# Kernel optimization log

Measured on AMD Instinct MI355X. Metric: run time of the kernel, lower is better.

Reference implementation:

```python
import jax, jax.numpy as jnp
import numpy as np
import math

S, B, D, H = 2048, 2, 1024, 16
DK = D // H

def setup_inputs() -> dict:
    key = jax.random.key(0)
    ks = jax.random.split(key, 32)
    f = lambda k, shape, s=1.0: jax.random.normal(k, shape, dtype=jnp.float32) * s
    inp = {
        'qx': f(ks[0], (S, B, D)),
        'kx': f(ks[1], (S, B, D)),
        'vx': f(ks[2], (S, B, D)),
        'qc': f(ks[3], (S, B, D)),
        'kc': f(ks[4], (S, B, D)),
    }
    w = 1.0 / math.sqrt(D)
    names = ['qx_lin', 'kx_lin', 'vx_lin', 'qc_lin', 'kc_lin', 'out_lin']
    for i, n in enumerate(names):
        inp['W_' + n] = f(ks[5 + 2 * i], (D, D), w)
        inp['b_' + n] = f(ks[6 + 2 * i], (D,), w)
    vnames = ['Vqx', 'Vqc', 'Vkx', 'Vkc']
    for i, n in enumerate(vnames):
        inp['W_' + n] = f(ks[17 + 2 * i], (D, 1), w)
        inp['b_' + n] = f(ks[18 + 2 * i], (1,), w)
    return inp

def _forward(qx, kx, vx, qc, kc,
             W_qx_lin, b_qx_lin, W_kx_lin, b_kx_lin, W_vx_lin, b_vx_lin,
             W_qc_lin, b_qc_lin, W_kc_lin, b_kc_lin, W_out_lin, b_out_lin,
             W_Vqx, b_Vqx, W_Vqc, b_Vqc, W_Vkx, b_Vkx, W_Vkc, b_Vkc):
    # [S,B,D] -> [B,S,D]
    qx = jnp.swapaxes(qx, 0, 1)
    kx = jnp.swapaxes(kx, 0, 1)
    vx = jnp.swapaxes(vx, 0, 1)
    qc = jnp.swapaxes(qc, 0, 1)
    kc = jnp.swapaxes(kc, 0, 1)
    bs = qx.shape[0]

    qx = qx @ W_qx_lin + b_qx_lin
    kx = kx @ W_kx_lin + b_kx_lin
    v = vx @ W_vx_lin + b_vx_lin
    qc = qc @ W_qc_lin + b_qc_lin
    kc = kc @ W_kc_lin + b_kc_lin

    lam_q = jax.nn.sigmoid((qx @ W_Vqx + b_Vqx) + (qc @ W_Vqc + b_Vqc))  # [B,S,1]
    lam_k = jax.nn.sigmoid((kx @ W_Vkx + b_Vkx) + (kc @ W_Vkc + b_Vkc))
    q = (1.0 - lam_q) * qx + lam_q * qc
    k = (1.0 - lam_k) * kx + lam_k * kc

    # [B,S,D] -> [B,H,S,dk]
    q = q.reshape(bs, -1, H, DK).transpose(0, 2, 1, 3)
    k = k.reshape(bs, -1, H, DK).transpose(0, 2, 1, 3)
    v = v.reshape(bs, -1, H, DK).transpose(0, 2, 1, 3)

    scores = jnp.einsum('bhqd,bhkd->bhqk', q, k) / math.sqrt(DK)
    attn = jax.nn.softmax(scores, axis=-1)  # dropout is identity in eval
    ctx = jnp.einsum('bhqk,bhkd->bhqd', attn, v)

    concat = ctx.transpose(0, 2, 1, 3).reshape(bs, -1, D)
    out = concat @ W_out_lin + b_out_lin
    return jnp.swapaxes(out, 0, 1)  # back to [S,B,D]

def reference(qx, kx, vx, qc, kc,
              W_qx_lin, b_qx_lin, W_kx_lin, b_kx_lin, W_vx_lin, b_vx_lin,
              W_qc_lin, b_qc_lin, W_kc_lin, b_kc_lin, W_out_lin, b_out_lin,
              W_Vqx, b_Vqx, W_Vqc, b_Vqc, W_Vkx, b_Vkx, W_Vkc, b_Vkc):
    return _forward(qx, kx, vx, qc, kc,
                    W_qx_lin, b_qx_lin, W_kx_lin, b_kx_lin, W_vx_lin, b_vx_lin,
                    W_qc_lin, b_qc_lin, W_kc_lin, b_kc_lin, W_out_lin, b_out_lin,
                    W_Vqx, b_Vqx, W_Vqc, b_Vqc, W_Vkx, b_Vkx, W_Vkc, b_Vkc)
```

## Files before the change

### kernel.cpp

```cpp
#include <hip/hip_runtime.h>
#include <math.h>

typedef unsigned short u16;
typedef __attribute__((ext_vector_type(8))) short short8;
typedef __attribute__((ext_vector_type(4))) float floatx4;
typedef __attribute__((ext_vector_type(4))) unsigned short ushort4v;
typedef __attribute__((ext_vector_type(2))) unsigned int uint2v;

__device__ __forceinline__ float bf2f(u16 x) {
    union { unsigned int u; float f; } v; v.u = ((unsigned int)x) << 16; return v.f;
}
__device__ __forceinline__ u16 f2bf(float f) {
    union { float f; unsigned int u; } v; v.f = f;
    unsigned int r = v.u + 0x7fffu + ((v.u >> 16) & 1u);
    return (u16)(r >> 16);
}
__device__ __forceinline__ unsigned int pk2bf(float a, float b) {
#if __has_builtin(__builtin_amdgcn_cvt_pk_bf16_f32)
    auto r = __builtin_amdgcn_cvt_pk_bf16_f32(a, b);
    union { decltype(r) v; unsigned int u; } cv; cv.v = r; return cv.u;
#else
    return (unsigned int)f2bf(a) | ((unsigned int)f2bf(b) << 16);
#endif
}

__device__ __forceinline__ void gl_lds16(const void* g, void* l) {
    __builtin_amdgcn_global_load_lds(
        (const __attribute__((address_space(1))) unsigned int*)g,
        (__attribute__((address_space(3))) unsigned int*)l,
        16, 0, 0);
}

struct WFuseJobs { const float* W[4]; const float* wv[4]; float* out[4]; };

__global__ __launch_bounds__(256) void wfuse(WFuseJobs wf) {
    const int z = blockIdx.y;
    const float* W = wf.W[z];
    const float* wv = wf.wv[z];
    float* out = wf.out[z];
    const int lane = threadIdx.x & 63, w = threadIdx.x >> 6;
#pragma unroll
    for (int i = 0; i < 4; i++) {
        const int row = blockIdx.x * 16 + w * 4 + i;
        const float* Wr = W + (size_t)row * 1024 + lane * 16;
        const float* vr = wv + lane * 16;
        float p = 0.f;
#pragma unroll
        for (int c = 0; c < 4; c++) {
            const floatx4 a = *(const floatx4*)(Wr + c * 4);
            const floatx4 b = *(const floatx4*)(vr + c * 4);
            p += a[0] * b[0] + a[1] * b[1] + a[2] * b[2] + a[3] * b[3];
        }
#pragma unroll
        for (int m = 1; m <= 32; m <<= 1) p += __shfl_xor(p, m);
        if (lane == 0) out[row] = p;
    }
}

struct CastJobs { const float* src[5]; u16* dst[5]; const float* w[5]; float* dot[5]; };

__global__ __launch_bounds__(256) void castbf(CastJobs cj) {
    const int z = blockIdx.y;
    const int row = blockIdx.x;
    const int t = threadIdx.x;
    const size_t i = (size_t)row * 256 + t;
    const floatx4 v = *(const floatx4*)(cj.src[z] + i * 4);
    ushort4v o;
#pragma unroll
    for (int j = 0; j < 4; j++) o[j] = f2bf(v[j]);
    *(ushort4v*)(cj.dst[z] + i * 4) = o;

    if (cj.w[z]) {
        const floatx4 wv = *(const floatx4*)(cj.w[z] + t * 4);
        float p = v[0] * wv[0] + v[1] * wv[1] + v[2] * wv[2] + v[3] * wv[3];
#pragma unroll
        for (int m = 1; m <= 32; m <<= 1) p += __shfl_xor(p, m);
        __shared__ float red[4];
        if ((t & 63) == 0) red[t >> 6] = p;
        __syncthreads();
        if (t == 0) cj.dot[z][row] = red[0] + red[1] + red[2] + red[3];
    }
}

struct LamJobs {
    const float* dA[2]; const float* dB[2];
    const float* b1[2]; const float* b2[2];
    const float* wv1[2]; const float* wv2[2];
    const float* s1[2]; const float* s2[2];
    float* lam[2];
};

__global__ __launch_bounds__(256) void lamk(LamJobs lj) {
    const int z = blockIdx.y;
    const int t = threadIdx.x;
    float p = 0.f;
    {
        const floatx4 a1 = *(const floatx4*)(lj.b1[z] + t * 4);
        const floatx4 w1 = *(const floatx4*)(lj.wv1[z] + t * 4);
        const floatx4 a2 = *(const floatx4*)(lj.b2[z] + t * 4);
        const floatx4 w2 = *(const floatx4*)(lj.wv2[z] + t * 4);
#pragma unroll
        for (int j = 0; j < 4; j++) p += a1[j] * w1[j] + a2[j] * w2[j];
    }
#pragma unroll
    for (int m = 1; m <= 32; m <<= 1) p += __shfl_xor(p, m);
    __shared__ float red[4];
    if ((t & 63) == 0) red[t >> 6] = p;
    __syncthreads();
    const float c = red[0] + red[1] + red[2] + red[3] + lj.s1[z][0] + lj.s2[z][0];
    const int row = blockIdx.x * 256 + t;
    const float x = lj.dA[z][row] + lj.dB[z][row] + c;
    lj.lam[z][row] = 1.f / (1.f + exp2f(-x * 1.44269504f));
}

struct WTJobs { const float* src[6]; u16* dst[6]; };

__global__ __launch_bounds__(256) void wtrans(WTJobs wj) {
    __shared__ float tile[32][33];
    const int z = blockIdx.z;
    const float* W = wj.src[z];
    u16* Wt = wj.dst[z];
    const int n0 = blockIdx.x * 32, k0 = blockIdx.y * 32;
    const int tx = threadIdx.x & 31, ty = threadIdx.x >> 5;
#pragma unroll
    for (int i = 0; i < 4; i++)
        tile[ty + i * 8][tx] = W[(size_t)(k0 + ty + i * 8) * 1024 + n0 + tx];
    __syncthreads();
#pragma unroll
    for (int i = 0; i < 4; i++)
        Wt[(size_t)(n0 + ty + i * 8) * 1024 + k0 + tx] = f2bf(tile[tx][ty + i * 8]);
}

__global__ __launch_bounds__(256) void vtrans(const u16* __restrict__ V,
                                              u16* __restrict__ Vtg) {
    __shared__ u16 tile[32][34];
    const int bh = blockIdx.z, b = bh >> 4, h = bh & 15;
    const int base = b * 1024 + h * 64;
    const int s0 = blockIdx.x * 32, d0 = blockIdx.y * 32;
    const int tx = threadIdx.x & 31, ty = threadIdx.x >> 5;
#pragma unroll
    for (int i = 0; i < 4; i++)
        tile[ty + i * 8][tx] = V[(size_t)(s0 + ty + i * 8) * 2048 + base + d0 + tx];
    __syncthreads();
#pragma unroll
    for (int i = 0; i < 4; i++)
        Vtg[((size_t)bh * 64 + d0 + ty + i * 8) * 2048 + s0 + tx] = tile[tx][ty + i * 8];
}

struct GemmJob { const u16* A; const u16* Bt; const float* bias; u16* Cb; float* Cf; };
struct GemmJobs { GemmJob j[1]; };

__global__ __launch_bounds__(256, 2) void gemm_bt(GemmJobs jobs, int K, int N, int f32out) {
    __shared__ u16 As[128 * 32];
    __shared__ u16 Bs[128 * 32];
    const GemmJob jb = jobs.j[blockIdx.z];
    const int m0 = blockIdx.y * 128;
    const int n0 = blockIdx.x * 128;
    const int t = threadIdx.x;
    const int lane = t & 63;
    const int wid = t >> 6;
    const int wm = wid >> 1, wn = wid & 1;
    const int qd = lane >> 4, lm = lane & 15;

    const floatx4 zero4 = {0.f, 0.f, 0.f, 0.f};
    floatx4 acc[4][4];
#pragma unroll
    for (int i = 0; i < 4; i++)
#pragma unroll
        for (int j2 = 0; j2 < 4; j2++) acc[i][j2] = zero4;

    const u16* Ab = jb.A + (size_t)m0 * K;
    const u16* Bb = jb.Bt + (size_t)n0 * K;
    const int e0 = t * 8;
    const int r0 = e0 >> 5, c0 = e0 & 31;
    const int e1 = (256 + t) * 8;
    const int r1 = e1 >> 5, c1 = e1 & 31;

    for (int k0 = 0; k0 < K; k0 += 32) {
        __syncthreads();
        gl_lds16(Ab + (size_t)r0 * K + k0 + c0, &As[e0]);
        gl_lds16(Ab + (size_t)r1 * K + k0 + c1, &As[e1]);
        gl_lds16(Bb + (size_t)r0 * K + k0 + c0, &Bs[e0]);
        gl_lds16(Bb + (size_t)r1 * K + k0 + c1, &Bs[e1]);
        __syncthreads();

        short8 af[4], bfg[4];
#pragma unroll
        for (int i = 0; i < 4; i++) {
            af[i]  = *(const short8*)&As[(wm * 64 + i * 16 + lm) * 32 + qd * 8];
            bfg[i] = *(const short8*)&Bs[(wn * 64 + i * 16 + lm) * 32 + qd * 8];
        }
#pragma unroll
        for (int i = 0; i < 4; i++)
#pragma unroll
            for (int j2 = 0; j2 < 4; j2++)
                acc[i][j2] = __builtin_amdgcn_mfma_f32_16x16x32_bf16(af[i], bfg[j2], acc[i][j2], 0, 0, 0);
    }

#pragma unroll
    for (int i = 0; i < 4; i++) {
        const int mb = m0 + wm * 64 + i * 16 + qd * 4;
#pragma unroll
        for (int j2 = 0; j2 < 4; j2++) {
            const int col = n0 + wn * 64 + j2 * 16 + lm;
            const float bv = jb.bias[col];
            const floatx4 c = acc[i][j2];
            if (f32out) {
#pragma unroll
                for (int r = 0; r < 4; r++)
                    jb.Cf[(size_t)(mb + r) * N + col] = c[r] + bv;
            } else {
#pragma unroll
                for (int r = 0; r < 4; r++)
                    jb.Cb[(size_t)(mb + r) * N + col] = f2bf(c[r] + bv);
            }
        }
    }
}

struct FuseJob {
    const u16* Aa; const u16* Ac; const u16* Ba; const u16* Bc;
    const float* biasA; const float* biasC; const float* lam; u16* out;
};
struct FuseJobs { FuseJob j[2]; };

__global__ __launch_bounds__(256, 2) void fusedproj(FuseJobs jobs) {
    __shared__ u16 Asa[128 * 32];
    __shared__ u16 Asc[128 * 32];
    __shared__ u16 Bsa[128 * 32];
    __shared__ u16 Bsc[128 * 32];
    const FuseJob jb = jobs.j[blockIdx.z];
    const int K = 1024;
    const int m0 = blockIdx.y * 128;
    const int n0 = blockIdx.x * 128;
    const int t = threadIdx.x;
    const int lane = t & 63;
    const int wid = t >> 6;
    const int wm = wid >> 1, wn = wid & 1;
    const int qd = lane >> 4, lm = lane & 15;

    const floatx4 zero4 = {0.f, 0.f, 0.f, 0.f};
    floatx4 accA[4][4], accC[4][4];
#pragma unroll
    for (int i = 0; i < 4; i++)
#pragma unroll
        for (int j2 = 0; j2 < 4; j2++) { accA[i][j2] = zero4; accC[i][j2] = zero4; }

    const u16* Aab = jb.Aa + (size_t)m0 * K;
    const u16* Acb = jb.Ac + (size_t)m0 * K;
    const u16* Bab = jb.Ba + (size_t)n0 * K;
    const u16* Bcb = jb.Bc + (size_t)n0 * K;
    const int e0 = t * 8;
    const int r0 = e0 >> 5, c0 = e0 & 31;
    const int e1 = (256 + t) * 8;
    const int r1 = e1 >> 5, c1 = e1 & 31;

    for (int k0 = 0; k0 < K; k0 += 32) {
        __syncthreads();
        gl_lds16(Aab + (size_t)r0 * K + k0 + c0, &Asa[e0]);
        gl_lds16(Aab + (size_t)r1 * K + k0 + c1, &Asa[e1]);
        gl_lds16(Acb + (size_t)r0 * K + k0 + c0, &Asc[e0]);
        gl_lds16(Acb + (size_t)r1 * K + k0 + c1, &Asc[e1]);
        gl_lds16(Bab + (size_t)r0 * K + k0 + c0, &Bsa[e0]);
        gl_lds16(Bab + (size_t)r1 * K + k0 + c1, &Bsa[e1]);
        gl_lds16(Bcb + (size_t)r0 * K + k0 + c0, &Bsc[e0]);
        gl_lds16(Bcb + (size_t)r1 * K + k0 + c1, &Bsc[e1]);
        __syncthreads();

        short8 aa[4], ac[4], ba[4], bc[4];
#pragma unroll
        for (int i = 0; i < 4; i++) {
            aa[i] = *(const short8*)&Asa[(wm * 64 + i * 16 + lm) * 32 + qd * 8];
            ac[i] = *(const short8*)&Asc[(wm * 64 + i * 16 + lm) * 32 + qd * 8];
            ba[i] = *(const short8*)&Bsa[(wn * 64 + i * 16 + lm) * 32 + qd * 8];
            bc[i] = *(const short8*)&Bsc[(wn * 64 + i * 16 + lm) * 32 + qd * 8];
        }
#pragma unroll
        for (int i = 0; i < 4; i++)
#pragma unroll
            for (int j2 = 0; j2 < 4; j2++) {
                accA[i][j2] = __builtin_amdgcn_mfma_f32_16x16x32_bf16(aa[i], ba[j2], accA[i][j2], 0, 0, 0);
                accC[i][j2] = __builtin_amdgcn_mfma_f32_16x16x32_bf16(ac[i], bc[j2], accC[i][j2], 0, 0, 0);
            }
    }

#pragma unroll
    for (int i = 0; i < 4; i++) {
        const int mb = m0 + wm * 64 + i * 16 + qd * 4;
        float lamv[4];
#pragma unroll
        for (int r = 0; r < 4; r++) lamv[r] = jb.lam[mb + r];
#pragma unroll
        for (int j2 = 0; j2 < 4; j2++) {
            const int col = n0 + wn * 64 + j2 * 16 + lm;
            const float bA = jb.biasA[col];
            const float bC = jb.biasC[col];
#pragma unroll
            for (int r = 0; r < 4; r++) {
                const float va = accA[i][j2][r] + bA;
                const float vc = accC[i][j2][r] + bC;
                jb.out[(size_t)(mb + r) * 1024 + col] = f2bf(va + lamv[r] * (vc - va));
            }
        }
    }
}

__global__ __launch_bounds__(256, 2) void attn3(
    const u16* __restrict__ Q, const u16* __restrict__ Kk,
    const u16* __restrict__ Vtg, float* __restrict__ ctxp,
    float* __restrict__ lp) {
    __shared__ u16 Ks[64 * 72];
    __shared__ u16 Vs[64 * 72];
    __shared__ u16 Ps[4 * 32 * 72];

    const int bh = blockIdx.y, b = bh >> 4, h = bh & 15;
    const int sp = blockIdx.z;
    const int base = b * 1024 + h * 64;
    const int t = threadIdx.x, lane = t & 63, w = t >> 6;
    const int qd = lane >> 4, lm = lane & 15;
    const int q0 = blockIdx.x * 128 + w * 32;

    short8 qf[2][2];
#pragma unroll
    for (int qh = 0; qh < 2; qh++) {
        const u16* qr = Q + (size_t)(q0 + qh * 16 + lm) * 2048 + base;
#pragma unroll
        for (int c = 0; c < 2; c++)
            qf[qh][c] = *(const short8*)(qr + c * 32 + qd * 8);
    }

    const floatx4 zero4 = {0.f, 0.f, 0.f, 0.f};
    floatx4 ctx[2][4];
#pragma unroll
    for (int qh = 0; qh < 2; qh++)
#pragma unroll
        for (int g = 0; g < 4; g++) ctx[qh][g] = zero4;
    float lpart[2] = {0.f, 0.f};

    u16* Pw = &Ps[w * 32 * 72];
    const float C = 0.18033688011112042f;

    const int sr = t >> 3, sc = (t & 7) * 8;
    const u16* ksrc = Kk + (size_t)(sp * 1024 + sr) * 2048 + base + sc;
    const u16* vsrc = Vtg + ((size_t)bh * 64 + sr) * 2048 + sp * 1024 + sc;
    u16* kdst0 = &Ks[sr * 72 + sc];
    u16* kdst1 = &Ks[(sr + 32) * 72 + sc];
    u16* vdst0 = &Vs[sr * 72 + sc];
    u16* vdst1 = &Vs[(sr + 32) * 72 + sc];

    for (int kt = 0; kt < 16; kt++) {
        __syncthreads();
        *(short8*)kdst0 = *(const short8*)ksrc;
        *(short8*)kdst1 = *(const short8*)(ksrc + (size_t)32 * 2048);
        *(short8*)vdst0 = *(const short8*)vsrc;
        *(short8*)vdst1 = *(const short8*)(vsrc + (size_t)32 * 2048);
        ksrc += (size_t)64 * 2048;
        vsrc += 64;
        __syncthreads();

#pragma unroll
        for (int g = 0; g < 4; g++) {
            const short8 kf0 = *(const short8*)&Ks[(g * 16 + lm) * 72 + qd * 8];
            const short8 kf1 = *(const short8*)&Ks[(g * 16 + lm) * 72 + 32 + qd * 8];
#pragma unroll
            for (int qh = 0; qh < 2; qh++) {
                floatx4 st = zero4;
                st = __builtin_amdgcn_mfma_f32_16x16x32_bf16(kf0, qf[qh][0], st, 0, 0, 0);
                st = __builtin_amdgcn_mfma_f32_16x16x32_bf16(kf1, qf[qh][1], st, 0, 0, 0);
                const float p0 = exp2f(st[0] * C);
                const float p1 = exp2f(st[1] * C);
                const float p2 = exp2f(st[2] * C);
                const float p3 = exp2f(st[3] * C);
                lpart[qh] += (p0 + p1) + (p2 + p3);
                uint2v pw;
                pw[0] = pk2bf(p0, p1);
                pw[1] = pk2bf(p2, p3);
                *(uint2v*)&Pw[(qh * 16 + lm) * 72 + g * 16 + qd * 4] = pw;
            }
        }

        short8 pa[2][2];
#pragma unroll
        for (int qh = 0; qh < 2; qh++)
#pragma unroll
            for (int c = 0; c < 2; c++)
                pa[qh][c] = *(const short8*)&Pw[(qh * 16 + lm) * 72 + c * 32 + qd * 8];
#pragma unroll
        for (int g = 0; g < 4; g++) {
            const short8 vb0 = *(const short8*)&Vs[(g * 16 + lm) * 72 + qd * 8];
            const short8 vb1 = *(const short8*)&Vs[(g * 16 + lm) * 72 + 32 + qd * 8];
#pragma unroll
            for (int qh = 0; qh < 2; qh++) {
                ctx[qh][g] = __builtin_amdgcn_mfma_f32_16x16x32_bf16(pa[qh][0], vb0, ctx[qh][g], 0, 0, 0);
                ctx[qh][g] = __builtin_amdgcn_mfma_f32_16x16x32_bf16(pa[qh][1], vb1, ctx[qh][g], 0, 0, 0);
            }
        }
    }

    float* cbase = ctxp + (size_t)sp * 4194304;
#pragma unroll
    for (int qh = 0; qh < 2; qh++) {
        float l = lpart[qh];
        l += __shfl_xor(l, 16);
        l += __shfl_xor(l, 32);
        if (lane < 16)
            lp[(size_t)sp * 65536 + bh * 2048 + q0 + qh * 16 + lane] = l;
#pragma unroll
        for (int r = 0; r < 4; r++) {
            const int srow = q0 + qh * 16 + qd * 4 + r;
            float* orow = cbase + (size_t)srow * 2048 + base;
#pragma unroll
            for (int g = 0; g < 4; g++)
                orow[g * 16 + lm] = ctx[qh][g][r];
        }
    }
}

__global__ __launch_bounds__(256) void merge(const float* __restrict__ ctxp,
                                             const float* __restrict__ lp,
                                             u16* __restrict__ out) {
    const size_t idx = ((size_t)blockIdx.x * 256 + threadIdx.x) * 4;
    const floatx4 a = *(const floatx4*)(ctxp + idx);
    const floatx4 c = *(const floatx4*)(ctxp + 4194304 + idx);
    const int srow = (int)(idx >> 11);
    const int rem = (int)(idx & 2047);
    const int bh = rem >> 6;
    const float l = lp[bh * 2048 + srow] + lp[65536 + bh * 2048 + srow];
    const float inv = 1.0f / l;
    ushort4v o;
    const unsigned int lo = pk2bf((a[0] + c[0]) * inv, (a[1] + c[1]) * inv);
    const unsigned int hi = pk2bf((a[2] + c[2]) * inv, (a[3] + c[3]) * inv);
    o[0] = (u16)(lo & 0xffff); o[1] = (u16)(lo >> 16);
    o[2] = (u16)(hi & 0xffff); o[3] = (u16)(hi >> 16);
    *(ushort4v*)(out + idx) = o;
}

extern "C" void kernel_launch(void* const* d_in, const int* in_sizes, int n_in,
                              void* d_out, int out_size, void* d_ws, size_t ws_size,
                              hipStream_t stream) {
    const float* qx = (const float*)d_in[0];
    const float* kx = (const float*)d_in[1];
    const float* vx = (const float*)d_in[2];
    const float* qc = (const float*)d_in[3];
    const float* kc = (const float*)d_in[4];
    const float* W_qx = (const float*)d_in[5];   const float* b_qx = (const float*)d_in[6];
    const float* W_kx = (const float*)d_in[7];   const float* b_kx = (const float*)d_in[8];
    const float* W_vx = (const float*)d_in[9];   const float* b_vx = (const float*)d_in[10];
    const float* W_qc = (const float*)d_in[11];  const float* b_qc = (const float*)d_in[12];
    const float* W_kc = (const float*)d_in[13];  const float* b_kc = (const float*)d_in[14];
    const float* W_out = (const float*)d_in[15]; const float* b_out = (const float*)d_in[16];
    const float* W_Vqx = (const float*)d_in[17]; const float* b_Vqx = (const float*)d_in[18];
    const float* W_Vqc = (const float*)d_in[19]; const float* b_Vqc = (const float*)d_in[20];
    const float* W_Vkx = (const float*)d_in[21]; const float* b_Vkx = (const float*)d_in[22];
    const float* W_Vkc = (const float*)d_in[23]; const float* b_Vkc = (const float*)d_in[24];

    char* ws = (char*)d_ws;
    const size_t NT = 4194304;
    const size_t MB = 1048576;
    u16* Xb[5];
    for (int i = 0; i < 5; i++) Xb[i] = (u16*)(ws + (size_t)i * NT * 2);
    u16* Wt[6];
    for (int i = 0; i < 6; i++) Wt[i] = (u16*)(ws + 40 * MB + (size_t)i * 2 * MB);
    u16* Pv    = (u16*)(ws + 52 * MB);
    u16* qg    = (u16*)(ws + 60 * MB);
    u16* kg    = (u16*)(ws + 68 * MB);
    u16* ctxbf = (u16*)(ws + 76 * MB);
    float* wfused = (float*)(ws + 84 * MB);
    float* dots   = (float*)(ws + 84 * MB + 16384);
    float* lam    = (float*)(ws + 84 * MB + 16384 + 65536);
    float* l_part = (float*)(ws + 84 * MB + 16384 + 65536 + 32768);
    float* ctxp = (float*)ws;
    u16* Vtg    = (u16*)(ws + 32 * MB);

    WFuseJobs wf;
    wf.W[0] = W_qx; wf.wv[0] = W_Vqx; wf.out[0] = wfused;
    wf.W[1] = W_qc; wf.wv[1] = W_Vqc; wf.out[1] = wfused + 1024;
    wf.W[2] = W_kx; wf.wv[2] = W_Vkx; wf.out[2] = wfused + 2048;
    wf.W[3] = W_kc; wf.wv[3] = W_Vkc; wf.out[3] = wfused + 3072;
    wfuse<<<dim3(64, 4), 256, 0, stream>>>(wf);

    CastJobs cj;
    const float* srcs[5] = {qx, kx, vx, qc, kc};
    for (int i = 0; i < 5; i++) { cj.src[i] = srcs[i]; cj.dst[i] = Xb[i]; cj.w[i] = nullptr; cj.dot[i] = nullptr; }
    cj.w[0] = wfused;        cj.dot[0] = dots;
    cj.w[3] = wfused + 1024; cj.dot[3] = dots + 4096;
    cj.w[1] = wfused + 2048; cj.dot[1] = dots + 8192;
    cj.w[4] = wfused + 3072; cj.dot[4] = dots + 12288;
    castbf<<<dim3(4096, 5), 256, 0, stream>>>(cj);

    LamJobs lj;
    lj.dA[0] = dots;        lj.dB[0] = dots + 4096;
    lj.b1[0] = b_qx; lj.b2[0] = b_qc; lj.wv1[0] = W_Vqx; lj.wv2[0] = W_Vqc;
    lj.s1[0] = b_Vqx; lj.s2[0] = b_Vqc; lj.lam[0] = lam;
    lj.dA[1] = dots + 8192; lj.dB[1] = dots + 12288;
    lj.b1[1] = b_kx; lj.b2[1] = b_kc; lj.wv1[1] = W_Vkx; lj.wv2[1] = W_Vkc;
    lj.s1[1] = b_Vkx; lj.s2[1] = b_Vkc; lj.lam[1] = lam + 4096;
    lamk<<<dim3(16, 2), 256, 0, stream>>>(lj);

    WTJobs wj;
    const float* wsrc[6] = {W_qx, W_kx, W_vx, W_qc, W_kc, W_out};
    for (int i = 0; i < 6; i++) { wj.src[i] = wsrc[i]; wj.dst[i] = Wt[i]; }
    wtrans<<<dim3(32, 32, 6), 256, 0, stream>>>(wj);

    FuseJobs fj;
    fj.j[0].Aa = Xb[0]; fj.j[0].Ac = Xb[3]; fj.j[0].Ba = Wt[0]; fj.j[0].Bc = Wt[3];
    fj.j[0].biasA = b_qx; fj.j[0].biasC = b_qc; fj.j[0].lam = lam;        fj.j[0].out = qg;
    fj.j[1].Aa = Xb[1]; fj.j[1].Ac = Xb[4]; fj.j[1].Ba = Wt[1]; fj.j[1].Bc = Wt[4];
    fj.j[1].biasA = b_kx; fj.j[1].biasC = b_kc; fj.j[1].lam = lam + 4096; fj.j[1].out = kg;
    fusedproj<<<dim3(8, 32, 2), 256, 0, stream>>>(fj);

    GemmJobs gv;
    gv.j[0].A = Xb[2]; gv.j[0].Bt = Wt[2]; gv.j[0].bias = b_vx;
    gv.j[0].Cb = Pv; gv.j[0].Cf = nullptr;
    gemm_bt<<<dim3(8, 32, 1), 256, 0, stream>>>(gv, 1024, 1024, 0);

    vtrans<<<dim3(64, 2, 32), 256, 0, stream>>>(Pv, Vtg);

    attn3<<<dim3(16, 32, 2), 256, 0, stream>>>(qg, kg, Vtg, ctxp, l_part);

    merge<<<4096, 256, 0, stream>>>(ctxp, l_part, ctxbf);

    GemmJobs gf;
    gf.j[0].A = ctxbf; gf.j[0].Bt = Wt[5]; gf.j[0].bias = b_out;
    gf.j[0].Cb = nullptr; gf.j[0].Cf = (float*)d_out;
    gemm_bt<<<dim3(8, 32, 1), 256, 0, stream>>>(gf, 1024, 1024, 1);
}
```

Measured before the change: 388.9 us.

## Merge projections into one launch, enlarge attention tiles, prefetch K/V, smaller output GEMM tiles

Folds the V projection GEMM into the fused Q/K projection kernel as a third grid slice, so one launch covers all input projections. The attention kernel now gives each wave 64 query rows instead of 32, halving the block count and reusing each K/V tile across more queries. It also prefetches the next K/V tile into registers while the current one is being computed. The output projection uses a 64-row-tile GEMM with 4 blocks per CU for better occupancy. The trade-offs are more registers per attention wave and a branch on job type inside the projection kernel.

```diff
diff --git a/kernel.cpp b/kernel.cpp
--- a/kernel.cpp
+++ b/kernel.cpp
@@ -147,89 +147,18 @@
         Vtg[((size_t)bh * 64 + d0 + ty + i * 8) * 2048 + s0 + tx] = tile[tx][ty + i * 8];
 }
 
-struct GemmJob { const u16* A; const u16* Bt; const float* bias; u16* Cb; float* Cf; };
-struct GemmJobs { GemmJob j[1]; };
-
-__global__ __launch_bounds__(256, 2) void gemm_bt(GemmJobs jobs, int K, int N, int f32out) {
-    __shared__ u16 As[128 * 32];
-    __shared__ u16 Bs[128 * 32];
-    const GemmJob jb = jobs.j[blockIdx.z];
-    const int m0 = blockIdx.y * 128;
-    const int n0 = blockIdx.x * 128;
-    const int t = threadIdx.x;
-    const int lane = t & 63;
-    const int wid = t >> 6;
-    const int wm = wid >> 1, wn = wid & 1;
-    const int qd = lane >> 4, lm = lane & 15;
-
-    const floatx4 zero4 = {0.f, 0.f, 0.f, 0.f};
-    floatx4 acc[4][4];
-#pragma unroll
-    for (int i = 0; i < 4; i++)
-#pragma unroll
-        for (int j2 = 0; j2 < 4; j2++) acc[i][j2] = zero4;
-
-    const u16* Ab = jb.A + (size_t)m0 * K;
-    const u16* Bb = jb.Bt + (size_t)n0 * K;
-    const int e0 = t * 8;
-    const int r0 = e0 >> 5, c0 = e0 & 31;
-    const int e1 = (256 + t) * 8;
-    const int r1 = e1 >> 5, c1 = e1 & 31;
-
-    for (int k0 = 0; k0 < K; k0 += 32) {
-        __syncthreads();
-        gl_lds16(Ab + (size_t)r0 * K + k0 + c0, &As[e0]);
-        gl_lds16(Ab + (size_t)r1 * K + k0 + c1, &As[e1]);
-        gl_lds16(Bb + (size_t)r0 * K + k0 + c0, &Bs[e0]);
-        gl_lds16(Bb + (size_t)r1 * K + k0 + c1, &Bs[e1]);
-        __syncthreads();
-
-        short8 af[4], bfg[4];
-#pragma unroll
-        for (int i = 0; i < 4; i++) {
-            af[i]  = *(const short8*)&As[(wm * 64 + i * 16 + lm) * 32 + qd * 8];
-            bfg[i] = *(const short8*)&Bs[(wn * 64 + i * 16 + lm) * 32 + qd * 8];
-        }
-#pragma unroll
-        for (int i = 0; i < 4; i++)
-#pragma unroll
-            for (int j2 = 0; j2 < 4; j2++)
-                acc[i][j2] = __builtin_amdgcn_mfma_f32_16x16x32_bf16(af[i], bfg[j2], acc[i][j2], 0, 0, 0);
-    }
-
-#pragma unroll
-    for (int i = 0; i < 4; i++) {
-        const int mb = m0 + wm * 64 + i * 16 + qd * 4;
-#pragma unroll
-        for (int j2 = 0; j2 < 4; j2++) {
-            const int col = n0 + wn * 64 + j2 * 16 + lm;
-            const float bv = jb.bias[col];
-            const floatx4 c = acc[i][j2];
-            if (f32out) {
-#pragma unroll
-                for (int r = 0; r < 4; r++)
-                    jb.Cf[(size_t)(mb + r) * N + col] = c[r] + bv;
-            } else {
-#pragma unroll
-                for (int r = 0; r < 4; r++)
-                    jb.Cb[(size_t)(mb + r) * N + col] = f2bf(c[r] + bv);
-            }
-        }
-    }
-}
-
-struct FuseJob {
+struct PJob {
     const u16* Aa; const u16* Ac; const u16* Ba; const u16* Bc;
     const float* biasA; const float* biasC; const float* lam; u16* out;
 };
-struct FuseJobs { FuseJob j[2]; };
-
-__global__ __launch_bounds__(256, 2) void fusedproj(FuseJobs jobs) {
+struct PJobs { PJob j[3]; };
+
+__global__ __launch_bounds__(256, 2) void projall(PJobs jobs) {
     __shared__ u16 Asa[128 * 32];
     __shared__ u16 Asc[128 * 32];
     __shared__ u16 Bsa[128 * 32];
     __shared__ u16 Bsc[128 * 32];
-    const FuseJob jb = jobs.j[blockIdx.z];
+    const PJob jb = jobs.j[blockIdx.z];
     const int K = 1024;
     const int m0 = blockIdx.y * 128;
     const int n0 = blockIdx.x * 128;
@@ -240,104 +169,211 @@
     const int qd = lane >> 4, lm = lane & 15;
 
     const floatx4 zero4 = {0.f, 0.f, 0.f, 0.f};
-    floatx4 accA[4][4], accC[4][4];
-#pragma unroll
-    for (int i = 0; i < 4; i++)
-#pragma unroll
-        for (int j2 = 0; j2 < 4; j2++) { accA[i][j2] = zero4; accC[i][j2] = zero4; }
-
-    const u16* Aab = jb.Aa + (size_t)m0 * K;
-    const u16* Acb = jb.Ac + (size_t)m0 * K;
-    const u16* Bab = jb.Ba + (size_t)n0 * K;
-    const u16* Bcb = jb.Bc + (size_t)n0 * K;
     const int e0 = t * 8;
     const int r0 = e0 >> 5, c0 = e0 & 31;
     const int e1 = (256 + t) * 8;
     const int r1 = e1 >> 5, c1 = e1 & 31;
 
+    const u16* Aab = jb.Aa + (size_t)m0 * K;
+    const u16* Bab = jb.Ba + (size_t)n0 * K;
+
+    if (jb.Ac) {
+        floatx4 accA[4][4], accC[4][4];
+#pragma unroll
+        for (int i = 0; i < 4; i++)
+#pragma unroll
+            for (int j2 = 0; j2 < 4; j2++) { accA[i][j2] = zero4; accC[i][j2] = zero4; }
+        const u16* Acb = jb.Ac + (size_t)m0 * K;
+        const u16* Bcb = jb.Bc + (size_t)n0 * K;
+
+        for (int k0 = 0; k0 < K; k0 += 32) {
+            __syncthreads();
+            gl_lds16(Aab + (size_t)r0 * K + k0 + c0, &Asa[e0]);
+            gl_lds16(Aab + (size_t)r1 * K + k0 + c1, &Asa[e1]);
+            gl_lds16(Acb + (size_t)r0 * K + k0 + c0, &Asc[e0]);
+            gl_lds16(Acb + (size_t)r1 * K + k0 + c1, &Asc[e1]);
+            gl_lds16(Bab + (size_t)r0 * K + k0 + c0, &Bsa[e0]);
+            gl_lds16(Bab + (size_t)r1 * K + k0 + c1, &Bsa[e1]);
+            gl_lds16(Bcb + (size_t)r0 * K + k0 + c0, &Bsc[e0]);
+            gl_lds16(Bcb + (size_t)r1 * K + k0 + c1, &Bsc[e1]);
+            __syncthreads();
+
+            short8 aa[4], ac[4], ba[4], bc[4];
+#pragma unroll
+            for (int i = 0; i < 4; i++) {
+                aa[i] = *(const short8*)&Asa[(wm * 64 + i * 16 + lm) * 32 + qd * 8];
+                ac[i] = *(const short8*)&Asc[(wm * 64 + i * 16 + lm) * 32 + qd * 8];
+                ba[i] = *(const short8*)&Bsa[(wn * 64 + i * 16 + lm) * 32 + qd * 8];
+                bc[i] = *(const short8*)&Bsc[(wn * 64 + i * 16 + lm) * 32 + qd * 8];
+            }
+#pragma unroll
+            for (int i = 0; i < 4; i++)
+#pragma unroll
+                for (int j2 = 0; j2 < 4; j2++) {
+                    accA[i][j2] = __builtin_amdgcn_mfma_f32_16x16x32_bf16(aa[i], ba[j2], accA[i][j2], 0, 0, 0);
+                    accC[i][j2] = __builtin_amdgcn_mfma_f32_16x16x32_bf16(ac[i], bc[j2], accC[i][j2], 0, 0, 0);
+                }
+        }
+
+#pragma unroll
+        for (int i = 0; i < 4; i++) {
+            const int mb = m0 + wm * 64 + i * 16 + qd * 4;
+            float lamv[4];
+#pragma unroll
+            for (int r = 0; r < 4; r++) lamv[r] = jb.lam[mb + r];
+#pragma unroll
+            for (int j2 = 0; j2 < 4; j2++) {
+                const int col = n0 + wn * 64 + j2 * 16 + lm;
+                const float bA = jb.biasA[col];
+                const float bC = jb.biasC[col];
+#pragma unroll
+                for (int r = 0; r < 4; r++) {
+                    const float va = accA[i][j2][r] + bA;
+                    const float vc = accC[i][j2][r] + bC;
+                    jb.out[(size_t)(mb + r) * 1024 + col] = f2bf(va + lamv[r] * (vc - va));
+                }
+            }
+        }
+    } else {
+        floatx4 acc[4][4];
+#pragma unroll
+        for (int i = 0; i < 4; i++)
+#pragma unroll
+            for (int j2 = 0; j2 < 4; j2++) acc[i][j2] = zero4;
+
+        for (int k0 = 0; k0 < K; k0 += 32) {
+            __syncthreads();
+            gl_lds16(Aab + (size_t)r0 * K + k0 + c0, &Asa[e0]);
+            gl_lds16(Aab + (size_t)r1 * K + k0 + c1, &Asa[e1]);
+            gl_lds16(Bab + (size_t)r0 * K + k0 + c0, &Bsa[e0]);
+            gl_lds16(Bab + (size_t)r1 * K + k0 + c1, &Bsa[e1]);
+            __syncthreads();
+
+            short8 af[4], bfg[4];
+#pragma unroll
+            for (int i = 0; i < 4; i++) {
+                af[i]  = *(const short8*)&Asa[(wm * 64 + i * 16 + lm) * 32 + qd * 8];
+                bfg[i] = *(const short8*)&Bsa[(wn * 64 + i * 16 + lm) * 32 + qd * 8];
+            }
+#pragma unroll
+            for (int i = 0; i < 4; i++)
+#pragma unroll
+                for (int j2 = 0; j2 < 4; j2++)
+                    acc[i][j2] = __builtin_amdgcn_mfma_f32_16x16x32_bf16(af[i], bfg[j2], acc[i][j2], 0, 0, 0);
+        }
+
+#pragma unroll
+        for (int i = 0; i < 4; i++) {
+            const int mb = m0 + wm * 64 + i * 16 + qd * 4;
+#pragma unroll
+            for (int j2 = 0; j2 < 4; j2++) {
+                const int col = n0 + wn * 64 + j2 * 16 + lm;
+                const float bv = jb.biasA[col];
+#pragma unroll
+                for (int r = 0; r < 4; r++)
+                    jb.out[(size_t)(mb + r) * 1024 + col] = f2bf(acc[i][j2][r] + bv);
+            }
+        }
+    }
+}
+
+__global__ __launch_bounds__(256, 4) void gemm64(const u16* __restrict__ A,
+                                                 const u16* __restrict__ Bt,
+                                                 const float* __restrict__ bias,
+                                                 float* __restrict__ C) {
+    __shared__ u16 As[64 * 32];
+    __shared__ u16 Bs[128 * 32];
+    const int K = 1024;
+    const int m0 = blockIdx.y * 64;
+    const int n0 = blockIdx.x * 128;
+    const int t = threadIdx.x;
+    const int lane = t & 63;
+    const int wid = t >> 6;
+    const int wm = wid >> 1, wn = wid & 1;
+    const int qd = lane >> 4, lm = lane & 15;
+
+    const floatx4 zero4 = {0.f, 0.f, 0.f, 0.f};
+    floatx4 acc[2][4];
+#pragma unroll
+    for (int i = 0; i < 2; i++)
+#pragma unroll
+        for (int j2 = 0; j2 < 4; j2++) acc[i][j2] = zero4;
+
+    const u16* Ab = A + (size_t)m0 * K;
+    const u16* Bb = Bt + (size_t)n0 * K;
+    const int e0 = t * 8;
+    const int r0 = e0 >> 5, c0 = e0 & 31;
+    const int e1 = (256 + t) * 8;
+    const int r1 = e1 >> 5, c1 = e1 & 31;
+
     for (int k0 = 0; k0 < K; k0 += 32) {
         __syncthreads();
-        gl_lds16(Aab + (size_t)r0 * K + k0 + c0, &Asa[e0]);
-        gl_lds16(Aab + (size_t)r1 * K + k0 + c1, &Asa[e1]);
-        gl_lds16(Acb + (size_t)r0 * K + k0 + c0, &Asc[e0]);
-        gl_lds16(Acb + (size_t)r1 * K + k0 + c1, &Asc[e1]);
-        gl_lds16(Bab + (size_t)r0 * K + k0 + c0, &Bsa[e0]);
-        gl_lds16(Bab + (size_t)r1 * K + k0 + c1, &Bsa[e1]);
-        gl_lds16(Bcb + (size_t)r0 * K + k0 + c0, &Bsc[e0]);
-        gl_lds16(Bcb + (size_t)r1 * K + k0 + c1, &Bsc[e1]);
+        gl_lds16(Ab + (size_t)r0 * K + k0 + c0, &As[e0]);
+        gl_lds16(Bb + (size_t)r0 * K + k0 + c0, &Bs[e0]);
+        gl_lds16(Bb + (size_t)r1 * K + k0 + c1, &Bs[e1]);
         __syncthreads();
 
-        short8 aa[4], ac[4], ba[4], bc[4];
-#pragma unroll
-        for (int i = 0; i < 4; i++) {
-            aa[i] = *(const short8*)&Asa[(wm * 64 + i * 16 + lm) * 32 + qd * 8];
-            ac[i] = *(const short8*)&Asc[(wm * 64 + i * 16 + lm) * 32 + qd * 8];
-            ba[i] = *(const short8*)&Bsa[(wn * 64 + i * 16 + lm) * 32 + qd * 8];
-            bc[i] = *(const short8*)&Bsc[(wn * 64 + i * 16 + lm) * 32 + qd * 8];
-        }
-#pragma unroll
-        for (int i = 0; i < 4; i++)
-#pragma unroll
-            for (int j2 = 0; j2 < 4; j2++) {
-                accA[i][j2] = __builtin_amdgcn_mfma_f32_16x16x32_bf16(aa[i], ba[j2], accA[i][j2], 0, 0, 0);
-                accC[i][j2] = __builtin_amdgcn_mfma_f32_16x16x32_bf16(ac[i], bc[j2], accC[i][j2], 0, 0, 0);
-            }
-    }
-
-#pragma unroll
-    for (int i = 0; i < 4; i++) {
-        const int mb = m0 + wm * 64 + i * 16 + qd * 4;
-        float lamv[4];
-#pragma unroll
-        for (int r = 0; r < 4; r++) lamv[r] = jb.lam[mb + r];
+        short8 af[2], bfg[4];
+#pragma unroll
+        for (int i = 0; i < 2; i++)
+            af[i] = *(const short8*)&As[(wm * 32 + i * 16 + lm) * 32 + qd * 8];
+#pragma unroll
+        for (int j2 = 0; j2 < 4; j2++)
+            bfg[j2] = *(const short8*)&Bs[(wn * 64 + j2 * 16 + lm) * 32 + qd * 8];
+#pragma unroll
+        for (int i = 0; i < 2; i++)
+#pragma unroll
+            for (int j2 = 0; j2 < 4; j2++)
+                acc[i][j2] = __builtin_amdgcn_mfma_f32_16x16x32_bf16(af[i], bfg[j2], acc[i][j2], 0, 0, 0);
+    }
+
+#pragma unroll
+    for (int i = 0; i < 2; i++) {
+        const int mb = m0 + wm * 32 + i * 16 + qd * 4;
 #pragma unroll
         for (int j2 = 0; j2 < 4; j2++) {
             const int col = n0 + wn * 64 + j2 * 16 + lm;
-            const float bA = jb.biasA[col];
-            const float bC = jb.biasC[col];
-#pragma unroll
-            for (int r = 0; r < 4; r++) {
-                const float va = accA[i][j2][r] + bA;
-                const float vc = accC[i][j2][r] + bC;
-                jb.out[(size_t)(mb + r) * 1024 + col] = f2bf(va + lamv[r] * (vc - va));
-            }
-        }
-    }
-}
-
-__global__ __launch_bounds__(256, 2) void attn3(
+            const float bv = bias[col];
+#pragma unroll
+            for (int r = 0; r < 4; r++)
+                C[(size_t)(mb + r) * 1024 + col] = acc[i][j2][r] + bv;
+        }
+    }
+}
+
+__global__ __launch_bounds__(256, 2) void attn4(
     const u16* __restrict__ Q, const u16* __restrict__ Kk,
     const u16* __restrict__ Vtg, float* __restrict__ ctxp,
     float* __restrict__ lp) {
     __shared__ u16 Ks[64 * 72];
     __shared__ u16 Vs[64 * 72];
-    __shared__ u16 Ps[4 * 32 * 72];
+    __shared__ u16 Ps[4 * 64 * 72];
 
     const int bh = blockIdx.y, b = bh >> 4, h = bh & 15;
     const int sp = blockIdx.z;
     const int base = b * 1024 + h * 64;
     const int t = threadIdx.x, lane = t & 63, w = t >> 6;
     const int qd = lane >> 4, lm = lane & 15;
-    const int q0 = blockIdx.x * 128 + w * 32;
-
-    short8 qf[2][2];
-#pragma unroll
-    for (int qh = 0; qh < 2; qh++) {
-        const u16* qr = Q + (size_t)(q0 + qh * 16 + lm) * 2048 + base;
+    const int q0w = blockIdx.x * 256 + w * 64;
+
+    short8 qf[4][2];
+#pragma unroll
+    for (int qh = 0; qh < 4; qh++) {
+        const u16* qr = Q + (size_t)(q0w + qh * 16 + lm) * 2048 + base;
 #pragma unroll
         for (int c = 0; c < 2; c++)
             qf[qh][c] = *(const short8*)(qr + c * 32 + qd * 8);
     }
 
     const floatx4 zero4 = {0.f, 0.f, 0.f, 0.f};
-    floatx4 ctx[2][4];
-#pragma unroll
-    for (int qh = 0; qh < 2; qh++)
+    floatx4 ctx[4][4];
+#pragma unroll
+    for (int qh = 0; qh < 4; qh++)
 #pragma unroll
         for (int g = 0; g < 4; g++) ctx[qh][g] = zero4;
-    float lpart[2] = {0.f, 0.f};
-
-    u16* Pw = &Ps[w * 32 * 72];
+    float lpart[4] = {0.f, 0.f, 0.f, 0.f};
+
+    u16* Pw = &Ps[w * 64 * 72];
     const float C = 0.18033688011112042f;
 
     const int sr = t >> 3, sc = (t & 7) * 8;
@@ -348,22 +384,33 @@
     u16* vdst0 = &Vs[sr * 72 + sc];
     u16* vdst1 = &Vs[(sr + 32) * 72 + sc];
 
+    short8 ka0 = *(const short8*)ksrc;
+    short8 ka1 = *(const short8*)(ksrc + (size_t)32 * 2048);
+    short8 va0 = *(const short8*)vsrc;
+    short8 va1 = *(const short8*)(vsrc + (size_t)32 * 2048);
+
     for (int kt = 0; kt < 16; kt++) {
         __syncthreads();
-        *(short8*)kdst0 = *(const short8*)ksrc;
-        *(short8*)kdst1 = *(const short8*)(ksrc + (size_t)32 * 2048);
-        *(short8*)vdst0 = *(const short8*)vsrc;
-        *(short8*)vdst1 = *(const short8*)(vsrc + (size_t)32 * 2048);
-        ksrc += (size_t)64 * 2048;
-        vsrc += 64;
+        *(short8*)kdst0 = ka0;
+        *(short8*)kdst1 = ka1;
+        *(short8*)vdst0 = va0;
+        *(short8*)vdst1 = va1;
         __syncthreads();
+        if (kt < 15) {
+            ksrc += (size_t)64 * 2048;
+            vsrc += 64;
+            ka0 = *(const short8*)ksrc;
+            ka1 = *(const short8*)(ksrc + (size_t)32 * 2048);
+            va0 = *(const short8*)vsrc;
+            va1 = *(const short8*)(vsrc + (size_t)32 * 2048);
+        }
 
 #pragma unroll
         for (int g = 0; g < 4; g++) {
             const short8 kf0 = *(const short8*)&Ks[(g * 16 + lm) * 72 + qd * 8];
             const short8 kf1 = *(const short8*)&Ks[(g * 16 + lm) * 72 + 32 + qd * 8];
 #pragma unroll
-            for (int qh = 0; qh < 2; qh++) {
+            for (int qh = 0; qh < 4; qh++) {
                 floatx4 st = zero4;
                 st = __builtin_amdgcn_mfma_f32_16x16x32_bf16(kf0, qf[qh][0], st, 0, 0, 0);
                 st = __builtin_amdgcn_mfma_f32_16x16x32_bf16(kf1, qf[qh][1], st, 0, 0, 0);
@@ -379,9 +426,9 @@
             }
         }
 
-        short8 pa[2][2];
-#pragma unroll
-        for (int qh = 0; qh < 2; qh++)
+        short8 pa[4][2];
+#pragma unroll
+        for (int qh = 0; qh < 4; qh++)
 #pragma unroll
             for (int c = 0; c < 2; c++)
                 pa[qh][c] = *(const short8*)&Pw[(qh * 16 + lm) * 72 + c * 32 + qd * 8];
@@ -390,7 +437,7 @@
             const short8 vb0 = *(const short8*)&Vs[(g * 16 + lm) * 72 + qd * 8];
             const short8 vb1 = *(const short8*)&Vs[(g * 16 + lm) * 72 + 32 + qd * 8];
 #pragma unroll
-            for (int qh = 0; qh < 2; qh++) {
+            for (int qh = 0; qh < 4; qh++) {
                 ctx[qh][g] = __builtin_amdgcn_mfma_f32_16x16x32_bf16(pa[qh][0], vb0, ctx[qh][g], 0, 0, 0);
                 ctx[qh][g] = __builtin_amdgcn_mfma_f32_16x16x32_bf16(pa[qh][1], vb1, ctx[qh][g], 0, 0, 0);
             }
@@ -399,15 +446,15 @@
 
     float* cbase = ctxp + (size_t)sp * 4194304;
 #pragma unroll
-    for (int qh = 0; qh < 2; qh++) {
+    for (int qh = 0; qh < 4; qh++) {
         float l = lpart[qh];
         l += __shfl_xor(l, 16);
         l += __shfl_xor(l, 32);
         if (lane < 16)
-            lp[(size_t)sp * 65536 + bh * 2048 + q0 + qh * 16 + lane] = l;
+            lp[(size_t)sp * 65536 + bh * 2048 + q0w + qh * 16 + lane] = l;
 #pragma unroll
         for (int r = 0; r < 4; r++) {
-            const int srow = q0 + qh * 16 + qd * 4 + r;
+            const int srow = q0w + qh * 16 + qd * 4 + r;
             float* orow = cbase + (size_t)srow * 2048 + base;
 #pragma unroll
             for (int g = 0; g < 4; g++)
@@ -502,26 +549,20 @@
     for (int i = 0; i < 6; i++) { wj.src[i] = wsrc[i]; wj.dst[i] = Wt[i]; }
     wtrans<<<dim3(32, 32, 6), 256, 0, stream>>>(wj);
 
-    FuseJobs fj;
-    fj.j[0].Aa = Xb[0]; fj.j[0].Ac = Xb[3]; fj.j[0].Ba = Wt[0]; fj.j[0].Bc = Wt[3];
-    fj.j[0].biasA = b_qx; fj.j[0].biasC = b_qc; fj.j[0].lam = lam;        fj.j[0].out = qg;
-    fj.j[1].Aa = Xb[1]; fj.j[1].Ac = Xb[4]; fj.j[1].Ba = Wt[1]; fj.j[1].Bc = Wt[4];
-    fj.j[1].biasA = b_kx; fj.j[1].biasC = b_kc; fj.j[1].lam = lam + 4096; fj.j[1].out = kg;
-    fusedproj<<<dim3(8, 32, 2), 256, 0, stream>>>(fj);
-
-    GemmJobs gv;
-    gv.j[0].A = Xb[2]; gv.j[0].Bt = Wt[2]; gv.j[0].bias = b_vx;
-    gv.j[0].Cb = Pv; gv.j[0].Cf = nullptr;
-    gemm_bt<<<dim3(8, 32, 1), 256, 0, stream>>>(gv, 1024, 1024, 0);
+    PJobs pj;
+    pj.j[0].Aa = Xb[0]; pj.j[0].Ac = Xb[3]; pj.j[0].Ba = Wt[0]; pj.j[0].Bc = Wt[3];
+    pj.j[0].biasA = b_qx; pj.j[0].biasC = b_qc; pj.j[0].lam = lam;        pj.j[0].out = qg;
+    pj.j[1].Aa = Xb[1]; pj.j[1].Ac = Xb[4]; pj.j[1].Ba = Wt[1]; pj.j[1].Bc = Wt[4];
+    pj.j[1].biasA = b_kx; pj.j[1].biasC = b_kc; pj.j[1].lam = lam + 4096; pj.j[1].out = kg;
+    pj.j[2].Aa = Xb[2]; pj.j[2].Ac = nullptr; pj.j[2].Ba = Wt[2]; pj.j[2].Bc = nullptr;
+    pj.j[2].biasA = b_vx; pj.j[2].biasC = nullptr; pj.j[2].lam = nullptr; pj.j[2].out = Pv;
+    projall<<<dim3(8, 32, 3), 256, 0, stream>>>(pj);
 
     vtrans<<<dim3(64, 2, 32), 256, 0, stream>>>(Pv, Vtg);
 
-    attn3<<<dim3(16, 32, 2), 256, 0, stream>>>(qg, kg, Vtg, ctxp, l_part);
+    attn4<<<dim3(8, 32, 2), 256, 0, stream>>>(qg, kg, Vtg, ctxp, l_part);
 
     merge<<<4096, 256, 0, stream>>>(ctxp, l_part, ctxbf);
 
-    GemmJobs gf;
-    gf.j[0].A = ctxbf; gf.j[0].Bt = Wt[5]; gf.j[0].bias = b_out;
-    gf.j[0].Cb = nullptr; gf.j[0].Cf = (float*)d_out;
-    gemm_bt<<<dim3(8, 32, 1), 256, 0, stream>>>(gf, 1024, 1024, 1);
-}
+    gemm64<<<dim3(8, 64), 256, 0, stream>>>(ctxbf, Wt[5], b_out, (float*)d_out);
+}
```

Result: faster. 366.8 us (-5.7%).
